# Performance work log

Measured on AMD Instinct MI355X. Metric: run time of the kernel, lower is better.

## Reference

```python
import jax, jax.numpy as jnp
import numpy as np

B, S, H = 1, 1024, 2048
NH, NKV, HD = 32, 4, 128
E, K, I = 32, 8, 768
EPS = 1e-6
THETA = 10000.0


def setup_inputs() -> dict:
    key = jax.random.key(0)
    ks = jax.random.split(key, 12)
    s = 0.02
    return {
        "x": jax.random.normal(ks[0], (B, S, H), jnp.float32),
        "ln1_w": jnp.ones((H,), jnp.float32),
        "ln2_w": jnp.ones((H,), jnp.float32),
        "q_norm_w": jnp.ones((HD,), jnp.float32),
        "k_norm_w": jnp.ones((HD,), jnp.float32),
        "Wq": jax.random.normal(ks[1], (H, NH * HD), jnp.float32) * s,
        "Wk": jax.random.normal(ks[2], (H, NKV * HD), jnp.float32) * s,
        "Wv": jax.random.normal(ks[3], (H, NKV * HD), jnp.float32) * s,
        "Wo": jax.random.normal(ks[4], (NH * HD, H), jnp.float32) * s,
        "Wg": jax.random.normal(ks[5], (H, E), jnp.float32) * s,
        "W_gate_up": jax.random.normal(ks[6], (E, H, 2 * I), jnp.float32) * s,
        "W_down": jax.random.normal(ks[7], (E, I, H), jnp.float32) * s,
    }


def rms_norm(x, w, eps=EPS):
    var = jnp.mean(jnp.square(x), axis=-1, keepdims=True)
    return x * jax.lax.rsqrt(var + eps) * w


def rotate_half(x):
    x1, x2 = jnp.split(x, 2, axis=-1)
    return jnp.concatenate([-x2, x1], axis=-1)


def rope_cos_sin(seq_len, dtype):
    inv_freq = 1.0 / (THETA ** (jnp.arange(0, HD, 2, dtype=jnp.float32) / HD))
    freqs = jnp.arange(seq_len, dtype=jnp.float32)[:, None] * inv_freq[None, :]
    emb = jnp.concatenate([freqs, freqs], axis=-1)  # [S, HD]
    return jnp.cos(emb).astype(dtype)[None, :, None, :], jnp.sin(emb).astype(dtype)[None, :, None, :]


def attention(h, q_norm_w, k_norm_w, Wq, Wk, Wv, Wo):
    b, s, _ = h.shape
    q = (h @ Wq).reshape(b, s, NH, HD)
    k = (h @ Wk).reshape(b, s, NKV, HD)
    v = (h @ Wv).reshape(b, s, NKV, HD)
    # Qwen3 per-head q/k RMSNorm
    q = rms_norm(q, q_norm_w)
    k = rms_norm(k, k_norm_w)
    cos, sin = rope_cos_sin(s, h.dtype)
    q = q * cos + rotate_half(q) * sin
    k = k * cos + rotate_half(k) * sin
    # GQA: repeat kv heads
    rep = NH // NKV
    k = jnp.repeat(k, rep, axis=2)
    v = jnp.repeat(v, rep, axis=2)
    scale = HD ** -0.5
    scores = jnp.einsum('bqhd,bkhd->bhqk', q, k) * scale
    mask = jnp.tril(jnp.ones((s, s), bool))
    scores = jnp.where(mask[None, None], scores, jnp.array(-1e9, scores.dtype))
    attn = jax.nn.softmax(scores, axis=-1)
    out = jnp.einsum('bhqk,bkhd->bqhd', attn, v).reshape(b, s, NH * HD)
    return out @ Wo


def moe(h, Wg, W_gate_up, W_down):
    b, s, _ = h.shape
    t = h.reshape(b * s, H)
    logits = t @ Wg                          # [T, E]
    probs = jax.nn.softmax(logits, axis=-1)
    weights, indices = jax.lax.top_k(probs, K)  # [T, K] (no renormalization, per TopKRouter)
    combine = jnp.sum(jax.nn.one_hot(indices, E, dtype=t.dtype) * weights[..., None], axis=1)  # [T, E]
    gu = jnp.einsum('th,ehf->etf', t, W_gate_up)     # [E, T, 2I]
    gate, up = jnp.split(gu, 2, axis=-1)
    act = jax.nn.silu(gate) * up                     # [E, T, I]
    y = jnp.einsum('eti,eih->eth', act, W_down)      # [E, T, H]
    out = jnp.einsum('eth,te->th', y, combine)
    return out.reshape(b, s, H)


def reference(x, ln1_w, ln2_w, q_norm_w, k_norm_w, Wq, Wk, Wv, Wo, Wg, W_gate_up, W_down):
    h = x + attention(rms_norm(x, ln1_w), q_norm_w, k_norm_w, Wq, Wk, Wv, Wo)
    out = h + moe(rms_norm(h, ln2_w), Wg, W_gate_up, W_down)
    return out
```

## Files before the change

kernel.cpp:

```cpp
#include <hip/hip_runtime.h>
#include <hip/hip_bf16.h>


#define T_TOK 1024
#define HDIM  2048
#define NHEAD 32
#define NKVH  4
#define HD    128
#define NEXP  32
#define TOPK  8
#define IDIM  768

typedef __hip_bfloat16 bf16;

__device__ __forceinline__ float ld1(const float* p, size_t i) { return p[i]; }
__device__ __forceinline__ float ld1(const bf16* p, size_t i) { return __bfloat162float(p[i]); }

__global__ void detect_kernel(const unsigned* __restrict__ ln1w_bits, int* __restrict__ flag) {
  if (threadIdx.x == 0) flag[0] = (ln1w_bits[0] == 0x3F803F80u) ? 1 : 0;
}

template <typename Tx, typename Tw>
__device__ __forceinline__ void rms_body(const Tx* __restrict__ x, const Tw* __restrict__ w,
                                         float* __restrict__ out, float* red) {
  int t = blockIdx.x;
  const Tx* row = x + (size_t)t * HDIM;
  float ss = 0.f;
  for (int h = threadIdx.x; h < HDIM; h += 256) {
    float v = ld1(row, h);
    ss += v * v;
  }
#pragma unroll
  for (int off = 32; off; off >>= 1) ss += __shfl_down(ss, off);
  if ((threadIdx.x & 63) == 0) red[threadIdx.x >> 6] = ss;
  __syncthreads();
  float inv = rsqrtf((red[0] + red[1] + red[2] + red[3]) / (float)HDIM + 1e-6f);
  float* o = out + (size_t)t * HDIM;
  for (int h = threadIdx.x; h < HDIM; h += 256) o[h] = ld1(row, h) * inv * ld1(w, h);
}

__global__ void rmsnorm_dyn_kernel(const void* x, const void* w, float* out, const int* flag) {
  __shared__ float red[4];
  if (flag[0]) rms_body<bf16, bf16>((const bf16*)x, (const bf16*)w, out, red);
  else         rms_body<float, float>((const float*)x, (const float*)w, out, red);
}

__global__ void rmsnorm_f32_kernel(const float* x, const void* w, float* out, const int* flag) {
  __shared__ float red[4];
  if (flag[0]) rms_body<float, bf16>(x, (const bf16*)w, out, red);
  else         rms_body<float, float>(x, (const float*)w, out, red);
}

template <typename Tb>
__device__ __forceinline__ void gemm_body(const float* __restrict__ A, const Tb* __restrict__ B,
                                          float* __restrict__ C, const Tb* __restrict__ res,
                                          int N, int K, float* As , float* Bs) {
  int tid = threadIdx.x;
  int tx = tid & 15, ty = tid >> 4;
  int row0 = blockIdx.y * 64, col0 = blockIdx.x * 64;
  float acc[4][4] = {};
  for (int k0 = 0; k0 < K; k0 += 16) {
#pragma unroll
    for (int l = 0; l < 4; ++l) {
      int idx = tid + l * 256;
      int r = idx >> 4, c = idx & 15;
      As[c * 65 + r] = A[(size_t)(row0 + r) * K + k0 + c];
    }
#pragma unroll
    for (int l = 0; l < 4; ++l) {
      int idx = tid + l * 256;
      int r = idx >> 6, c = idx & 63;
      Bs[r * 65 + c] = ld1(B, (size_t)(k0 + r) * N + col0 + c);
    }
    __syncthreads();
#pragma unroll
    for (int k = 0; k < 16; ++k) {
      float av[4], bv[4];
#pragma unroll
      for (int i = 0; i < 4; ++i) av[i] = As[k * 65 + ty * 4 + i];
#pragma unroll
      for (int j = 0; j < 4; ++j) bv[j] = Bs[k * 65 + tx * 4 + j];
#pragma unroll
      for (int i = 0; i < 4; ++i)
#pragma unroll
        for (int j = 0; j < 4; ++j) acc[i][j] += av[i] * bv[j];
    }
    __syncthreads();
  }
#pragma unroll
  for (int i = 0; i < 4; ++i) {
    int r = row0 + ty * 4 + i;
#pragma unroll
    for (int j = 0; j < 4; ++j) {
      int c = col0 + tx * 4 + j;
      float v = acc[i][j];
      if (res) v += ld1(res, (size_t)r * N + c);
      C[(size_t)r * N + c] = v;
    }
  }
}

__global__ void gemm_kernel(const float* A, const void* B, float* C, const void* res,
                            int N, int K, const int* flag) {
  __shared__ float As[16 * 65];
  __shared__ float Bs[16 * 65];
  if (flag[0]) gemm_body<bf16>(A, (const bf16*)B, C, (const bf16*)res, N, K, As, Bs);
  else         gemm_body<float>(A, (const float*)B, C, (const float*)res, N, K, As, Bs);
}

template <typename Tw>
__device__ __forceinline__ void qkrope_body(float* __restrict__ q, float* __restrict__ k,
                                            const Tw* __restrict__ qw, const Tw* __restrict__ kw,
                                            float* sred, float* sh) {
  int t = blockIdx.x;
  int head = blockIdx.y;
  float* vec;
  const Tw* w;
  if (head < NHEAD) {
    vec = q + ((size_t)t * NHEAD + head) * HD;
    w = qw;
  } else {
    vec = k + ((size_t)t * NKVH + (head - NHEAD)) * HD;
    w = kw;
  }
  int d = threadIdx.x;
  float v = vec[d];
  float ss = v * v;
#pragma unroll
  for (int off = 32; off; off >>= 1) ss += __shfl_down(ss, off);
  if ((d & 63) == 0) sred[d >> 6] = ss;
  __syncthreads();
  float inv = rsqrtf((sred[0] + sred[1]) / (float)HD + 1e-6f);
  float nv = v * inv * ld1(w, d);
  sh[d] = nv;
  __syncthreads();
  float other = (d < 64) ? -sh[d + 64] : sh[d - 64];
  float inv_freq = powf(10000.f, -(float)(d & 63) / 64.f);
  float ang = (float)t * inv_freq;
  vec[d] = nv * cosf(ang) + other * sinf(ang);
}

__global__ void qk_norm_rope_kernel(float* q, float* k, const void* qw, const void* kw,
                                    const int* flag) {
  __shared__ float sred[2];
  __shared__ float sh[HD];
  if (flag[0]) qkrope_body<bf16>(q, k, (const bf16*)qw, (const bf16*)kw, sred, sh);
  else         qkrope_body<float>(q, k, (const float*)qw, (const float*)kw, sred, sh);
}

__global__ void attn_kernel(const float* __restrict__ q, const float* __restrict__ k,
                            const float* __restrict__ v, float* __restrict__ out) {
  int qi = blockIdx.x;
  int h = blockIdx.y;
  int kvh = h >> 3;
  int d = threadIdx.x;
  __shared__ __align__(16) float qv[HD];
  __shared__ float sc[128];
  __shared__ float redmax[2];
  __shared__ float redsum[2];
  qv[d] = q[((size_t)qi * NHEAD + h) * HD + d] * 0.08838834764831845f;
  __syncthreads();
  float m = -1e30f, l = 0.f, acc = 0.f;
  for (int j0 = 0; j0 <= qi; j0 += 128) {
    int nk = min(128, qi + 1 - j0);
    float s = -1e30f;
    if (d < nk) {
      const float4* q4 = reinterpret_cast<const float4*>(qv);
      const float4* k4 = reinterpret_cast<const float4*>(k + ((size_t)(j0 + d) * NKVH + kvh) * HD);
      float dot = 0.f;
#pragma unroll 8
      for (int e = 0; e < 32; ++e) {
        float4 a = q4[e], b = k4[e];
        dot += a.x * b.x + a.y * b.y + a.z * b.z + a.w * b.w;
      }
      s = dot;
    }
    float tm = s;
#pragma unroll
    for (int off = 32; off; off >>= 1) tm = fmaxf(tm, __shfl_down(tm, off));
    __syncthreads();
    if ((d & 63) == 0) redmax[d >> 6] = tm;
    __syncthreads();
    float newm = fmaxf(m, fmaxf(redmax[0], redmax[1]));
    float p = (d < nk) ? expf(s - newm) : 0.f;
    sc[d] = p;
    float ps = p;
#pragma unroll
    for (int off = 32; off; off >>= 1) ps += __shfl_down(ps, off);
    if ((d & 63) == 0) redsum[d >> 6] = ps;
    float corr = expf(m - newm);
    m = newm;
    __syncthreads();
    l = l * corr + redsum[0] + redsum[1];
    acc *= corr;
    const float* vp = v + ((size_t)j0 * NKVH + kvh) * HD + d;
    for (int j = 0; j < nk; ++j) acc += sc[j] * vp[(size_t)j * (NKVH * HD)];
  }
  out[(size_t)qi * (NHEAD * HD) + h * HD + d] = acc / l;
}

template <typename Tw>
__device__ __forceinline__ void router_body(const float* __restrict__ h2,
                                            const Tw* __restrict__ Wg,
                                            float* __restrict__ combine,
                                            float* sh, float* probs) {
  int t = blockIdx.x;
  for (int h = threadIdx.x; h < HDIM; h += 64) sh[h] = h2[(size_t)t * HDIM + h];
  __syncthreads();
  int e = threadIdx.x;
  if (e < NEXP) {
    float acc = 0.f;
    for (int h = 0; h < HDIM; ++h) acc += sh[h] * ld1(Wg, (size_t)h * NEXP + e);
    probs[e] = acc;
  }
  __syncthreads();
  if (threadIdx.x == 0) {
    float mx = -1e30f;
    for (int i = 0; i < NEXP; ++i) mx = fmaxf(mx, probs[i]);
    float p[NEXP], sum = 0.f;
    for (int i = 0; i < NEXP; ++i) {
      p[i] = expf(probs[i] - mx);
      sum += p[i];
    }
    float o[NEXP];
    for (int i = 0; i < NEXP; ++i) {
      p[i] /= sum;
      o[i] = 0.f;
    }
    for (int kk = 0; kk < TOPK; ++kk) {
      int arg = 0;
      float best = p[0];
      for (int i = 1; i < NEXP; ++i)
        if (p[i] > best) { best = p[i]; arg = i; }
      o[arg] = best;
      p[arg] = -1.f;
    }
    for (int i = 0; i < NEXP; ++i) combine[(size_t)t * NEXP + i] = o[i];
  }
}

__global__ void router_kernel(const float* h2, const void* Wg, float* combine, const int* flag) {
  __shared__ float sh[HDIM];
  __shared__ float probs[NEXP];
  if (flag[0]) router_body<bf16>(h2, (const bf16*)Wg, combine, sh, probs);
  else         router_body<float>(h2, (const float*)Wg, combine, sh, probs);
}

__global__ void gather_kernel(const float* __restrict__ comb, int* __restrict__ cnt,
                              int* __restrict__ tok) {
  int e = blockIdx.x;
  __shared__ int lcnt;
  if (threadIdx.x == 0) lcnt = 0;
  __syncthreads();
  for (int t = threadIdx.x; t < T_TOK; t += 256) {
    if (comb[(size_t)t * NEXP + e] != 0.f) {
      int slot = atomicAdd(&lcnt, 1);
      tok[e * T_TOK + slot] = t;
    }
  }
  __syncthreads();
  if (threadIdx.x == 0) cnt[e] = lcnt;
}

__global__ void scan_kernel(const int* __restrict__ cnt, int* __restrict__ off) {
  if (threadIdx.x == 0) {
    int s = 0;
    for (int e = 0; e < NEXP; ++e) { off[e] = s; s += cnt[e]; }
  }
}

template <typename Tw>
__device__ __forceinline__ void gu_body(const float* __restrict__ h2, const Tw* __restrict__ Wgu,
                                        const int* __restrict__ cnt, const int* __restrict__ off,
                                        const int* __restrict__ tok, float* __restrict__ act,
                                        float* As, float* Bg, float* Bu, int* stok) {
  int e = blockIdx.z;
  int cn = cnt[e];
  int m0 = blockIdx.y * 64;
  if (m0 >= cn) return;
  int col0 = blockIdx.x * 64;
  int tid = threadIdx.x;
  if (tid < 64) stok[tid] = (m0 + tid < cn) ? tok[e * T_TOK + m0 + tid] : tok[e * T_TOK];
  __syncthreads();
  int tx = tid & 15, ty = tid >> 4;
  const Tw* wg = Wgu + (size_t)e * HDIM * (2 * IDIM);
  float ag[4][4] = {}, au[4][4] = {};
  for (int k0 = 0; k0 < HDIM; k0 += 16) {
#pragma unroll
    for (int l = 0; l < 4; ++l) {
      int idx = tid + l * 256;
      int r = idx >> 4, c = idx & 15;
      As[c * 65 + r] = h2[(size_t)stok[r] * HDIM + k0 + c];
    }
#pragma unroll
    for (int l = 0; l < 4; ++l) {
      int idx = tid + l * 256;
      int r = idx >> 6, c = idx & 63;
      const Tw* rowp = wg + (size_t)(k0 + r) * (2 * IDIM) + col0 + c;
      Bg[r * 65 + c] = ld1(rowp, 0);
      Bu[r * 65 + c] = ld1(rowp, IDIM);
    }
    __syncthreads();
#pragma unroll
    for (int k = 0; k < 16; ++k) {
      float av[4], bg[4], bu[4];
#pragma unroll
      for (int i = 0; i < 4; ++i) av[i] = As[k * 65 + ty * 4 + i];
#pragma unroll
      for (int j = 0; j < 4; ++j) { bg[j] = Bg[k * 65 + tx * 4 + j]; bu[j] = Bu[k * 65 + tx * 4 + j]; }
#pragma unroll
      for (int i = 0; i < 4; ++i)
#pragma unroll
        for (int j = 0; j < 4; ++j) { ag[i][j] += av[i] * bg[j]; au[i][j] += av[i] * bu[j]; }
    }
    __syncthreads();
  }
  int arow0 = off[e] + m0;
#pragma unroll
  for (int i = 0; i < 4; ++i) {
    int lr = ty * 4 + i;
    if (m0 + lr >= cn) continue;
    float* arow = act + (size_t)(arow0 + lr) * IDIM + col0;
#pragma unroll
    for (int j = 0; j < 4; ++j) {
      float g = ag[i][j], u = au[i][j];
      arow[tx * 4 + j] = (g / (1.f + expf(-g))) * u;
    }
  }
}

__global__ void moe_gu_kernel(const float* h2, const void* Wgu, const int* cnt, const int* off,
                              const int* tok, float* act, const int* flag) {
  __shared__ float As[16 * 65];
  __shared__ float Bg[16 * 65];
  __shared__ float Bu[16 * 65];
  __shared__ int stok[64];
  if (flag[0]) gu_body<bf16>(h2, (const bf16*)Wgu, cnt, off, tok, act, As, Bg, Bu, stok);
  else         gu_body<float>(h2, (const float*)Wgu, cnt, off, tok, act, As, Bg, Bu, stok);
}

template <typename Tw>
__device__ __forceinline__ void down_body(const float* __restrict__ act, const Tw* __restrict__ Wd,
                                          const float* __restrict__ comb,
                                          const int* __restrict__ cnt, const int* __restrict__ off,
                                          const int* __restrict__ tok, float* __restrict__ moeb,
                                          float* As, float* Bs, int* stok) {
  int e = blockIdx.z;
  int cn = cnt[e];
  int m0 = blockIdx.y * 64;
  if (m0 >= cn) return;
  int col0 = blockIdx.x * 64;
  int tid = threadIdx.x;
  if (tid < 64) stok[tid] = (m0 + tid < cn) ? tok[e * T_TOK + m0 + tid] : tok[e * T_TOK];
  __syncthreads();
  int tx = tid & 15, ty = tid >> 4;
  const Tw* wd = Wd + (size_t)e * IDIM * HDIM;
  const float* Ae = act + (size_t)(off[e] + m0) * IDIM;
  float acc[4][4] = {};
  for (int k0 = 0; k0 < IDIM; k0 += 16) {
#pragma unroll
    for (int l = 0; l < 4; ++l) {
      int idx = tid + l * 256;
      int r = idx >> 4, c = idx & 15;
      As[c * 65 + r] = (m0 + r < cn) ? Ae[(size_t)r * IDIM + k0 + c] : 0.f;
    }
#pragma unroll
    for (int l = 0; l < 4; ++l) {
      int idx = tid + l * 256;
      int r = idx >> 6, c = idx & 63;
      Bs[r * 65 + c] = ld1(wd, (size_t)(k0 + r) * HDIM + col0 + c);
    }
    __syncthreads();
#pragma unroll
    for (int k = 0; k < 16; ++k) {
      float av[4], bv[4];
#pragma unroll
      for (int i = 0; i < 4; ++i) av[i] = As[k * 65 + ty * 4 + i];
#pragma unroll
      for (int j = 0; j < 4; ++j) bv[j] = Bs[k * 65 + tx * 4 + j];
#pragma unroll
      for (int i = 0; i < 4; ++i)
#pragma unroll
        for (int j = 0; j < 4; ++j) acc[i][j] += av[i] * bv[j];
    }
    __syncthreads();
  }
#pragma unroll
  for (int i = 0; i < 4; ++i) {
    int lr = ty * 4 + i;
    if (m0 + lr >= cn) continue;
    int t = stok[lr];
    float wgt = comb[(size_t)t * NEXP + e];
#pragma unroll
    for (int j = 0; j < 4; ++j)
      atomicAdd(&moeb[(size_t)t * HDIM + col0 + tx * 4 + j], wgt * acc[i][j]);
  }
}

__global__ void moe_down_kernel(const float* act, const void* Wd, const float* comb,
                                const int* cnt, const int* off, const int* tok,
                                float* moeb, const int* flag) {
  __shared__ float As[16 * 65];
  __shared__ float Bs[16 * 65];
  __shared__ int stok[64];
  if (flag[0]) down_body<bf16>(act, (const bf16*)Wd, comb, cnt, off, tok, moeb, As, Bs, stok);
  else         down_body<float>(act, (const float*)Wd, comb, cnt, off, tok, moeb, As, Bs, stok);
}

template <typename Tw>
__device__ __forceinline__ void moe_body(const float* __restrict__ h2, const Tw* __restrict__ Wgu,
                                         const Tw* __restrict__ Wd, const float* __restrict__ combine,
                                         float* __restrict__ moe_out, float* sh, float* act) {
  int t = blockIdx.x;
  int e = blockIdx.y;
  float wgt = combine[(size_t)t * NEXP + e];
  if (wgt == 0.f) return;
  int tid = threadIdx.x;
  for (int h = tid; h < HDIM; h += 256) sh[h] = h2[(size_t)t * HDIM + h];
  __syncthreads();
  const Tw* wg = Wgu + (size_t)e * HDIM * (2 * IDIM);
#pragma unroll
  for (int c = 0; c < 3; ++c) {
    int i = c * 256 + tid;
    float g = 0.f, u = 0.f;
    for (int h = 0; h < HDIM; ++h) {
      const Tw* rowp = wg + (size_t)h * (2 * IDIM);
      float hv = sh[h];
      g += hv * ld1(rowp, i);
      u += hv * ld1(rowp, i + IDIM);
    }
    act[i] = (g / (1.f + expf(-g))) * u;
  }
  __syncthreads();
  const Tw* wd = Wd + (size_t)e * IDIM * HDIM;
#pragma unroll
  for (int c = 0; c < 8; ++c) {
    int h = c * 256 + tid;
    float acc = 0.f;
    for (int i = 0; i < IDIM; ++i) acc += act[i] * ld1(wd, (size_t)i * HDIM + h);
    atomicAdd(&moe_out[(size_t)t * HDIM + h], wgt * acc);
  }
}

__global__ void moe_kernel(const float* h2, const void* Wgu, const void* Wd,
                           const float* combine, float* moe_out, const int* flag) {
  __shared__ float sh[HDIM];
  __shared__ float act[IDIM];
  if (flag[0]) moe_body<bf16>(h2, (const bf16*)Wgu, (const bf16*)Wd, combine, moe_out, sh, act);
  else         moe_body<float>(h2, (const float*)Wgu, (const float*)Wd, combine, moe_out, sh, act);
}

__global__ void final_add_kernel(const float* __restrict__ hres, const float* __restrict__ moe,
                                 void* __restrict__ out, const int* flag) {
  size_t i = (size_t)blockIdx.x * 256 + threadIdx.x;
  float v = hres[i] + moe[i];
  if (flag[0]) ((bf16*)out)[i] = __float2bfloat16(v);
  else         ((float*)out)[i] = v;
}

extern "C" void kernel_launch(void* const* d_in, const int* in_sizes, int n_in,
                              void* d_out, int out_size, void* d_ws, size_t ws_size,
                              hipStream_t stream) {
  const void* x        = d_in[0];
  const void* ln1_w    = d_in[1];
  const void* ln2_w    = d_in[2];
  const void* q_norm_w = d_in[3];
  const void* k_norm_w = d_in[4];
  const void* Wq       = d_in[5];
  const void* Wk       = d_in[6];
  const void* Wv       = d_in[7];
  const void* Wo       = d_in[8];
  const void* Wg       = d_in[9];
  const void* Wgu      = d_in[10];
  const void* Wd       = d_in[11];

  int* flag   = (int*)d_ws;
  float* base = (float*)((char*)d_ws + 16);
  float* h1   = base;
  float* qbuf = h1 + (size_t)T_TOK * HDIM;
  float* kbuf = qbuf + (size_t)T_TOK * NHEAD * HD;
  float* vbuf = kbuf + (size_t)T_TOK * NKVH * HD;
  float* h2   = qbuf;
  float* comb = qbuf + (size_t)T_TOK * HDIM;
  float* moeb = comb + (size_t)T_TOK * NEXP;
  int*   cnt  = (int*)vbuf;
  int*   offp = cnt + 32;
  int*   tok  = cnt + 128;
  float* act  = vbuf + (size_t)T_TOK * NKVH * HD;

  size_t need = 16 + sizeof(float) * ((size_t)T_TOK * HDIM + (size_t)T_TOK * NHEAD * HD +
                                      2 * (size_t)T_TOK * NKVH * HD +
                                      (size_t)T_TOK * TOPK * IDIM);
  bool grouped = ws_size >= need;

  detect_kernel<<<1, 64, 0, stream>>>((const unsigned*)ln1_w, flag);
  rmsnorm_dyn_kernel<<<T_TOK, 256, 0, stream>>>(x, ln1_w, h1, flag);
  gemm_kernel<<<dim3(NHEAD * HD / 64, T_TOK / 64), 256, 0, stream>>>(h1, Wq, qbuf, nullptr, NHEAD * HD, HDIM, flag);
  gemm_kernel<<<dim3(NKVH * HD / 64, T_TOK / 64), 256, 0, stream>>>(h1, Wk, kbuf, nullptr, NKVH * HD, HDIM, flag);
  gemm_kernel<<<dim3(NKVH * HD / 64, T_TOK / 64), 256, 0, stream>>>(h1, Wv, vbuf, nullptr, NKVH * HD, HDIM, flag);
  qk_norm_rope_kernel<<<dim3(T_TOK, NHEAD + NKVH), HD, 0, stream>>>(qbuf, kbuf, q_norm_w, k_norm_w, flag);
  attn_kernel<<<dim3(T_TOK, NHEAD), 128, 0, stream>>>(qbuf, kbuf, vbuf, qbuf);
  gemm_kernel<<<dim3(HDIM / 64, T_TOK / 64), 256, 0, stream>>>(qbuf, Wo, h1, x, HDIM, NHEAD * HD, flag);
  rmsnorm_f32_kernel<<<T_TOK, 256, 0, stream>>>(h1, ln2_w, h2, flag);
  hipMemsetAsync(moeb, 0, (size_t)T_TOK * HDIM * sizeof(float), stream);
  router_kernel<<<T_TOK, 64, 0, stream>>>(h2, Wg, comb, flag);
  if (grouped) {
    gather_kernel<<<NEXP, 256, 0, stream>>>(comb, cnt, tok);
    scan_kernel<<<1, 64, 0, stream>>>(cnt, offp);
    moe_gu_kernel<<<dim3(IDIM / 64, T_TOK / 64, NEXP), 256, 0, stream>>>(h2, Wgu, cnt, offp, tok, act, flag);
    moe_down_kernel<<<dim3(HDIM / 64, T_TOK / 64, NEXP), 256, 0, stream>>>(act, Wd, comb, cnt, offp, tok, moeb, flag);
  } else {
    moe_kernel<<<dim3(T_TOK, NEXP), 256, 0, stream>>>(h2, Wgu, Wd, comb, moeb, flag);
  }
  final_add_kernel<<<T_TOK * HDIM / 256, 256, 0, stream>>>(h1, moeb, d_out, flag);
}
```

Baseline: 4.930 ms.

## Replace per-query attention with tiled flash-attention kernel and causal load balancing

Replaces the one-block-per-query attention kernel with a 64x64 tiled flash-attention kernel that stages Q, K and V tiles in shared memory and keeps per-thread 4x8 output tiles in registers. Each block handles a pair of query tiles (p and 15-p) to balance the causal triangle. This cuts redundant global K/V reads across queries, but launches only 256 blocks, which may underfill the GPU. It also writes output in place over the q buffer, which is safe only because each block reads and writes only its own query rows and head columns.

```diff
diff --git a/kernel.cpp b/kernel.cpp
--- a/kernel.cpp
+++ b/kernel.cpp
@@ -148,55 +148,139 @@
   else         qkrope_body<float>(q, k, (const float*)qw, (const float*)kw, sred, sh);
 }
 
-__global__ void attn_kernel(const float* __restrict__ q, const float* __restrict__ k,
-                            const float* __restrict__ v, float* __restrict__ out) {
-  int qi = blockIdx.x;
-  int h = blockIdx.y;
+__global__ __launch_bounds__(256) void attn_tile_kernel(const float* q, const float* __restrict__ k,
+                                                        const float* __restrict__ v, float* out) {
+  __shared__ float Qs[64 * 132];
+  __shared__ float KVs[64 * 132];
+  int bid = blockIdx.x;
+  int h = bid & 31;
+  int p = bid >> 5;
   int kvh = h >> 3;
-  int d = threadIdx.x;
-  __shared__ __align__(16) float qv[HD];
-  __shared__ float sc[128];
-  __shared__ float redmax[2];
-  __shared__ float redsum[2];
-  qv[d] = q[((size_t)qi * NHEAD + h) * HD + d] * 0.08838834764831845f;
-  __syncthreads();
-  float m = -1e30f, l = 0.f, acc = 0.f;
-  for (int j0 = 0; j0 <= qi; j0 += 128) {
-    int nk = min(128, qi + 1 - j0);
-    float s = -1e30f;
-    if (d < nk) {
-      const float4* q4 = reinterpret_cast<const float4*>(qv);
-      const float4* k4 = reinterpret_cast<const float4*>(k + ((size_t)(j0 + d) * NKVH + kvh) * HD);
-      float dot = 0.f;
-#pragma unroll 8
-      for (int e = 0; e < 32; ++e) {
-        float4 a = q4[e], b = k4[e];
-        dot += a.x * b.x + a.y * b.y + a.z * b.z + a.w * b.w;
+  int tid = threadIdx.x;
+  int tx = tid & 15, ty = tid >> 4;
+  int laneband = tid & 48;
+  const float scale = 0.08838834764831845f;
+
+  for (int half = 0; half < 2; ++half) {
+    int qt = half ? (15 - p) : p;
+    int q0 = qt * 64;
+#pragma unroll
+    for (int l = 0; l < 8; ++l) {
+      int i = tid + l * 256;
+      int r = i >> 5, c4 = (i & 31) * 4;
+      float4 qv = *(const float4*)(q + (size_t)(q0 + r) * (NHEAD * HD) + h * HD + c4);
+      qv.x *= scale; qv.y *= scale; qv.z *= scale; qv.w *= scale;
+      *(float4*)&Qs[r * 132 + c4] = qv;
+    }
+    float m4[4] = {-1e30f, -1e30f, -1e30f, -1e30f};
+    float l4[4] = {};
+    float o[4][8] = {};
+    __syncthreads();
+
+    for (int kt = 0; kt <= qt; ++kt) {
+      int j0 = kt * 64;
+#pragma unroll
+      for (int l = 0; l < 8; ++l) {
+        int i = tid + l * 256;
+        int r = i >> 5, c4 = (i & 31) * 4;
+        *(float4*)&KVs[r * 132 + c4] =
+            *(const float4*)(k + (size_t)(j0 + r) * (NKVH * HD) + kvh * HD + c4);
       }
-      s = dot;
-    }
-    float tm = s;
-#pragma unroll
-    for (int off = 32; off; off >>= 1) tm = fmaxf(tm, __shfl_down(tm, off));
-    __syncthreads();
-    if ((d & 63) == 0) redmax[d >> 6] = tm;
-    __syncthreads();
-    float newm = fmaxf(m, fmaxf(redmax[0], redmax[1]));
-    float p = (d < nk) ? expf(s - newm) : 0.f;
-    sc[d] = p;
-    float ps = p;
-#pragma unroll
-    for (int off = 32; off; off >>= 1) ps += __shfl_down(ps, off);
-    if ((d & 63) == 0) redsum[d >> 6] = ps;
-    float corr = expf(m - newm);
-    m = newm;
-    __syncthreads();
-    l = l * corr + redsum[0] + redsum[1];
-    acc *= corr;
-    const float* vp = v + ((size_t)j0 * NKVH + kvh) * HD + d;
-    for (int j = 0; j < nk; ++j) acc += sc[j] * vp[(size_t)j * (NKVH * HD)];
-  }
-  out[(size_t)qi * (NHEAD * HD) + h * HD + d] = acc / l;
+      __syncthreads();
+      float s[4][4] = {};
+#pragma unroll 4
+      for (int d4 = 0; d4 < 32; ++d4) {
+        float4 av[4], bv[4];
+#pragma unroll
+        for (int i = 0; i < 4; ++i) av[i] = *(const float4*)&Qs[(ty + 16 * i) * 132 + d4 * 4];
+#pragma unroll
+        for (int j = 0; j < 4; ++j) bv[j] = *(const float4*)&KVs[(tx + 16 * j) * 132 + d4 * 4];
+#pragma unroll
+        for (int i = 0; i < 4; ++i)
+#pragma unroll
+          for (int j = 0; j < 4; ++j)
+            s[i][j] += av[i].x * bv[j].x + av[i].y * bv[j].y + av[i].z * bv[j].z + av[i].w * bv[j].w;
+      }
+      if (kt == qt) {
+#pragma unroll
+        for (int i = 0; i < 4; ++i)
+#pragma unroll
+          for (int j = 0; j < 4; ++j)
+            if (tx + 16 * j > ty + 16 * i) s[i][j] = -1e30f;
+      }
+      float rm[4], rs[4];
+#pragma unroll
+      for (int i = 0; i < 4; ++i)
+        rm[i] = fmaxf(fmaxf(s[i][0], s[i][1]), fmaxf(s[i][2], s[i][3]));
+#pragma unroll
+      for (int mm = 1; mm < 16; mm <<= 1)
+#pragma unroll
+        for (int i = 0; i < 4; ++i) rm[i] = fmaxf(rm[i], __shfl_xor(rm[i], mm));
+#pragma unroll
+      for (int i = 0; i < 4; ++i) {
+        float mn = fmaxf(m4[i], rm[i]);
+        float corr = __expf(m4[i] - mn);
+        m4[i] = mn;
+        rs[i] = 0.f;
+#pragma unroll
+        for (int j = 0; j < 4; ++j) {
+          s[i][j] = __expf(s[i][j] - mn);
+          rs[i] += s[i][j];
+        }
+        l4[i] *= corr;
+#pragma unroll
+        for (int c = 0; c < 8; ++c) o[i][c] *= corr;
+      }
+#pragma unroll
+      for (int mm = 1; mm < 16; mm <<= 1)
+#pragma unroll
+        for (int i = 0; i < 4; ++i) rs[i] += __shfl_xor(rs[i], mm);
+#pragma unroll
+      for (int i = 0; i < 4; ++i) l4[i] += rs[i];
+      __syncthreads();
+#pragma unroll
+      for (int l = 0; l < 8; ++l) {
+        int i = tid + l * 256;
+        int r = i >> 5, c4 = (i & 31) * 4;
+        *(float4*)&KVs[r * 132 + c4] =
+            *(const float4*)(v + (size_t)(j0 + r) * (NKVH * HD) + kvh * HD + c4);
+      }
+      __syncthreads();
+#pragma unroll
+      for (int j = 0; j < 4; ++j) {
+#pragma unroll 4
+        for (int kks = 0; kks < 16; ++kks) {
+          int kk = j * 16 + kks;
+          int src = laneband | kks;
+          float pb0 = __shfl(s[0][j], src);
+          float pb1 = __shfl(s[1][j], src);
+          float pb2 = __shfl(s[2][j], src);
+          float pb3 = __shfl(s[3][j], src);
+          float4 v0 = *(const float4*)&KVs[kk * 132 + tx * 8];
+          float4 v1 = *(const float4*)&KVs[kk * 132 + tx * 8 + 4];
+          o[0][0] += pb0 * v0.x; o[0][1] += pb0 * v0.y; o[0][2] += pb0 * v0.z; o[0][3] += pb0 * v0.w;
+          o[0][4] += pb0 * v1.x; o[0][5] += pb0 * v1.y; o[0][6] += pb0 * v1.z; o[0][7] += pb0 * v1.w;
+          o[1][0] += pb1 * v0.x; o[1][1] += pb1 * v0.y; o[1][2] += pb1 * v0.z; o[1][3] += pb1 * v0.w;
+          o[1][4] += pb1 * v1.x; o[1][5] += pb1 * v1.y; o[1][6] += pb1 * v1.z; o[1][7] += pb1 * v1.w;
+          o[2][0] += pb2 * v0.x; o[2][1] += pb2 * v0.y; o[2][2] += pb2 * v0.z; o[2][3] += pb2 * v0.w;
+          o[2][4] += pb2 * v1.x; o[2][5] += pb2 * v1.y; o[2][6] += pb2 * v1.z; o[2][7] += pb2 * v1.w;
+          o[3][0] += pb3 * v0.x; o[3][1] += pb3 * v0.y; o[3][2] += pb3 * v0.z; o[3][3] += pb3 * v0.w;
+          o[3][4] += pb3 * v1.x; o[3][5] += pb3 * v1.y; o[3][6] += pb3 * v1.z; o[3][7] += pb3 * v1.w;
+        }
+      }
+      __syncthreads();
+    }
+#pragma unroll
+    for (int i = 0; i < 4; ++i) {
+      float inv = 1.f / l4[i];
+      int row = q0 + ty + 16 * i;
+      float4 w0 = {o[i][0] * inv, o[i][1] * inv, o[i][2] * inv, o[i][3] * inv};
+      float4 w1 = {o[i][4] * inv, o[i][5] * inv, o[i][6] * inv, o[i][7] * inv};
+      *(float4*)(out + (size_t)row * (NHEAD * HD) + h * HD + tx * 8) = w0;
+      *(float4*)(out + (size_t)row * (NHEAD * HD) + h * HD + tx * 8 + 4) = w1;
+    }
+    __syncthreads();
+  }
 }
 
 template <typename Tw>
@@ -499,7 +583,7 @@
   gemm_kernel<<<dim3(NKVH * HD / 64, T_TOK / 64), 256, 0, stream>>>(h1, Wk, kbuf, nullptr, NKVH * HD, HDIM, flag);
   gemm_kernel<<<dim3(NKVH * HD / 64, T_TOK / 64), 256, 0, stream>>>(h1, Wv, vbuf, nullptr, NKVH * HD, HDIM, flag);
   qk_norm_rope_kernel<<<dim3(T_TOK, NHEAD + NKVH), HD, 0, stream>>>(qbuf, kbuf, q_norm_w, k_norm_w, flag);
-  attn_kernel<<<dim3(T_TOK, NHEAD), 128, 0, stream>>>(qbuf, kbuf, vbuf, qbuf);
+  attn_tile_kernel<<<256, 256, 0, stream>>>(qbuf, kbuf, vbuf, qbuf);
   gemm_kernel<<<dim3(HDIM / 64, T_TOK / 64), 256, 0, stream>>>(qbuf, Wo, h1, x, HDIM, NHEAD * HD, flag);
   rmsnorm_f32_kernel<<<T_TOK, 256, 0, stream>>>(h1, ln2_w, h2, flag);
   hipMemsetAsync(moeb, 0, (size_t)T_TOK * HDIM * sizeof(float), stream);
```

After: 3.991 ms. 19.0% less time.
